# Kernel tuning notes

Measured on AMD Instinct MI355X. Metric: run time of the kernel, lower is better.

## Reference

```python
import jax, jax.numpy as jnp
import numpy as np

B, IN_DIM, UNITS = 16384, 3072, 3072  # batch, input_dim=3*unit1, units=3*unit2


def setup_inputs() -> dict:
    key = jax.random.key(0)
    k1, k2, k3 = jax.random.split(key, 3)
    inputs = jax.random.normal(k1, (B, IN_DIM), dtype=jnp.float32)
    # original init: uniform [0, 0.01) for w, zeros for b (gpe_bias = [0, 0])
    w = jax.random.uniform(k2, (IN_DIM, UNITS), dtype=jnp.float32, minval=0.0, maxval=0.01)
    b = jnp.zeros((UNITS,), dtype=jnp.float32)
    # per-unit binary diagonal mask, stored as [units, input_dim]
    mask = jax.random.randint(k3, (UNITS, IN_DIM), 0, 2, dtype=jnp.int32)
    return {"inputs": inputs, "w": w, "b": b, "mask": mask}


def reference(inputs, w, b, mask):
    # Original: p = transpose(s @ inputs^T, [2,0,1]) -> [batch, units, input_dim]
    #           f = diag_part(p @ w) + b            -> [batch, units]
    # Since s[u] = diag(mask[u]), this is exactly:
    #   f[b,u] = sum_i inputs[b,i] * mask[u,i] * w[i,u] + b[u]
    # i.e. a single masked GEMM with effective weight w * mask^T.
    w_eff = w * mask.T.astype(w.dtype)  # [input_dim, units]
    return inputs @ w_eff + b
```

## Files before the change

kernel.cpp:

```cpp
#include <hip/hip_runtime.h>

#define BATCH 16384
#define KDIM  3072
#define NDIM  3072

typedef __bf16 bf16;
typedef bf16  bf16x8  __attribute__((ext_vector_type(8)));
typedef float f32x16  __attribute__((ext_vector_type(16)));

__device__ __forceinline__ void g2l16(const bf16* g, bf16* l) {
    __builtin_amdgcn_global_load_lds(
        (__attribute__((address_space(1))) unsigned int*)g,
        (__attribute__((address_space(3))) unsigned int*)l,
        16, 0, 0);
}

__global__ __launch_bounds__(256) void cvt_a_kernel(const float* __restrict__ in,
                                                    bf16* __restrict__ out) {
    const long idx = (long)blockIdx.x * 256 + threadIdx.x;
    const float4* in4 = (const float4*)in;
    float4 a = in4[idx * 2];
    float4 b = in4[idx * 2 + 1];
    bf16x8 o;
    o[0] = (bf16)a.x; o[1] = (bf16)a.y; o[2] = (bf16)a.z; o[3] = (bf16)a.w;
    o[4] = (bf16)b.x; o[5] = (bf16)b.y; o[6] = (bf16)b.z; o[7] = (bf16)b.w;
    ((bf16x8*)out)[idx] = o;
}

__global__ __launch_bounds__(256) void weff_kernel(const float* __restrict__ w,
                                                   const int* __restrict__ mask,
                                                   bf16* __restrict__ wt) {
    __shared__ float tile[32][33];
    const int i0 = blockIdx.x * 32;
    const int u0 = blockIdx.y * 32;
    const int tx = threadIdx.x, ty = threadIdx.y;
#pragma unroll
    for (int r = 0; r < 4; r++)
        tile[ty + 8 * r][tx] = w[(long)(i0 + ty + 8 * r) * NDIM + u0 + tx];
    __syncthreads();
#pragma unroll
    for (int r = 0; r < 4; r++) {
        int u = u0 + ty + 8 * r;
        int i = i0 + tx;
        float v = tile[tx][ty + 8 * r] * (float)mask[(long)u * KDIM + i];
        wt[(long)u * KDIM + i] = (bf16)v;
    }
}

__global__ __launch_bounds__(256, 2) void gemm_kernel(const bf16* __restrict__ A,
                                                      const bf16* __restrict__ Bt,
                                                      const float* __restrict__ bias,
                                                      float* __restrict__ C) {
    __shared__ __align__(16) bf16 lds[2 * 12288];

    const int tid  = threadIdx.x;
    const int lane = tid & 63;
    const int wv   = tid >> 6;
    const long m0 = (long)blockIdx.y * 256;
    const long n0 = (long)blockIdx.x * 128;
    const int waveM = (wv >> 1) * 128;
    const int waveN = (wv & 1) * 64;

    const int srow   = tid >> 2;
    const int schunk = tid & 3;
    const bf16* gA = A + (m0 + srow) * KDIM + schunk * 8;
    const bf16* gB = Bt + (n0 + srow) * KDIM + schunk * 8;

    const int rl = lane & 31;
    const int kb = lane >> 5;
    const int aBase = (waveM + rl) * 32 + kb * 8;
    const int bBase = 8192 + (waveN + rl) * 32 + kb * 8;

    f32x16 acc[4][2] = {};

    {
        bf16* d = &lds[tid * 8];
#pragma unroll
        for (int j = 0; j < 4; j++) g2l16(gA + (long)(64 * j) * KDIM, d + j * 2048);
#pragma unroll
        for (int j = 0; j < 2; j++) g2l16(gB + (long)(64 * j) * KDIM, d + 8192 + j * 2048);
    }
    __syncthreads();

    for (int i = 0; i < KDIM / 32; ++i) {
        const int p = i & 1;
        if (i + 1 < KDIM / 32) {
            const long ko = (long)(i + 1) * 32;
            bf16* d = &lds[(1 - p) * 12288 + tid * 8];
#pragma unroll
            for (int j = 0; j < 4; j++) g2l16(gA + (long)(64 * j) * KDIM + ko, d + j * 2048);
#pragma unroll
            for (int j = 0; j < 2; j++) g2l16(gB + (long)(64 * j) * KDIM + ko, d + 8192 + j * 2048);
        }

        const bf16* bp = &lds[p * 12288];
#pragma unroll
        for (int t = 0; t < 2; t++) {
            bf16x8 a[4], b[2];
#pragma unroll
            for (int mi = 0; mi < 4; mi++)
                a[mi] = *(const bf16x8*)(bp + aBase + mi * 1024 + t * 16);
#pragma unroll
            for (int ni = 0; ni < 2; ni++)
                b[ni] = *(const bf16x8*)(bp + bBase + ni * 1024 + t * 16);
#pragma unroll
            for (int mi = 0; mi < 4; mi++)
#pragma unroll
                for (int ni = 0; ni < 2; ni++)
                    acc[mi][ni] = __builtin_amdgcn_mfma_f32_32x32x16_bf16(
                        a[mi], b[ni], acc[mi][ni], 0, 0, 0);
        }
        __syncthreads();
    }

#pragma unroll
    for (int mi = 0; mi < 4; mi++) {
#pragma unroll
        for (int ni = 0; ni < 2; ni++) {
            const long col   = n0 + waveN + ni * 32 + rl;
            const long rbase = m0 + waveM + mi * 32 + 4 * kb;
            const float bv = bias[col];
#pragma unroll
            for (int g = 0; g < 4; g++)
#pragma unroll
                for (int t = 0; t < 4; t++)
                    C[(rbase + 8 * g + t) * NDIM + col] = acc[mi][ni][4 * g + t] + bv;
        }
    }
}

__global__ __launch_bounds__(256) void naive_kernel(const float* __restrict__ x,
                                                    const float* __restrict__ w,
                                                    const float* __restrict__ bias,
                                                    const int* __restrict__ mask,
                                                    float* __restrict__ out) {
    const long idx = (long)blockIdx.x * 256 + threadIdx.x;
    const long bi = idx / NDIM;
    const int u = (int)(idx % NDIM);
    float s = 0.f;
    for (int k = 0; k < KDIM; k++)
        s += x[bi * KDIM + k] * w[(long)k * NDIM + u] * (float)mask[(long)u * KDIM + k];
    out[idx] = s + bias[u];
}

extern "C" void kernel_launch(void* const* d_in, const int* in_sizes, int n_in,
                              void* d_out, int out_size, void* d_ws, size_t ws_size,
                              hipStream_t stream) {
    const float* x    = (const float*)d_in[0];
    const float* w    = (const float*)d_in[1];
    const float* bias = (const float*)d_in[2];
    const int*   mask = (const int*)d_in[3];
    float* out = (float*)d_out;

    const size_t needA = (size_t)BATCH * KDIM * sizeof(bf16);
    const size_t needW = (size_t)NDIM * KDIM * sizeof(bf16);

    if (ws_size < needA + needW) {
        const long total = (long)BATCH * NDIM;
        naive_kernel<<<(int)(total / 256), 256, 0, stream>>>(x, w, bias, mask, out);
        return;
    }

    bf16* Abf = (bf16*)d_ws;
    bf16* Wt  = (bf16*)((char*)d_ws + needA);

    cvt_a_kernel<<<(BATCH * (KDIM / 8)) / 256, 256, 0, stream>>>(x, Abf);
    weff_kernel<<<dim3(KDIM / 32, NDIM / 32), dim3(32, 8), 0, stream>>>(w, mask, Wt);
    gemm_kernel<<<dim3(NDIM / 128, BATCH / 256), 256, 0, stream>>>(Abf, Wt, bias, out);
}
```

Measured before the change: 697.0 us.

## Enlarge GEMM tile to 256x256 with swizzled LDS, K=64 stages and XCD remap

The GEMM kernel moves to 512-thread blocks computing 256x256 output tiles with BK=64. Each tile is double-buffered in 128KB of LDS, with XOR-swizzled layout to avoid bank conflicts. Fragment loads are register double-buffered across k-substeps, MFMA issue runs under raised priority, and manual vmcnt waits plus barriers replace __syncthreads. Block ids are remapped so consecutive tiles spread across XCDs for better L2 reuse. The larger tile cuts global/LDS traffic per flop, but the LDS footprint limits occupancy to one block per CU despite launch bounds asking for two.

```diff
diff --git a/kernel.cpp b/kernel.cpp
--- a/kernel.cpp
+++ b/kernel.cpp
@@ -47,83 +47,119 @@
     }
 }
 
-__global__ __launch_bounds__(256, 2) void gemm_kernel(const bf16* __restrict__ A,
+__global__ __launch_bounds__(512, 2) void gemm_kernel(const bf16* __restrict__ A,
                                                       const bf16* __restrict__ Bt,
                                                       const float* __restrict__ bias,
                                                       float* __restrict__ C) {
-    __shared__ __align__(16) bf16 lds[2 * 12288];
+    __shared__ __align__(16) bf16 lds[2 * 32768];
 
     const int tid  = threadIdx.x;
     const int lane = tid & 63;
     const int wv   = tid >> 6;
-    const long m0 = (long)blockIdx.y * 256;
-    const long n0 = (long)blockIdx.x * 128;
-    const int waveM = (wv >> 1) * 128;
-    const int waveN = (wv & 1) * 64;
-
-    const int srow   = tid >> 2;
-    const int schunk = tid & 3;
-    const bf16* gA = A + (m0 + srow) * KDIM + schunk * 8;
-    const bf16* gB = Bt + (n0 + srow) * KDIM + schunk * 8;
-
-    const int rl = lane & 31;
-    const int kb = lane >> 5;
-    const int aBase = (waveM + rl) * 32 + kb * 8;
-    const int bBase = 8192 + (waveN + rl) * 32 + kb * 8;
+    const int rl   = lane & 31;
+    const int kb   = lane >> 5;
+    const int sx   = rl & 7;
+
+    const int lid = blockIdx.y * gridDim.x + blockIdx.x;
+    const int sid = (lid & 7) * 96 + (lid >> 3);
+    const long m0 = (long)(sid / 12) * 256;
+    const long n0 = (long)(sid % 12) * 256;
+
+    const int waveM = (wv >> 2) * 128;
+    const int waveN = (wv & 3) * 64;
+
+    const int srow = tid >> 3;
+    const int sc   = (tid & 7) ^ (srow & 7);
+    const bf16* gA = A  + (m0 + srow) * KDIM + sc * 8;
+    const bf16* gB = Bt + (n0 + srow) * KDIM + sc * 8;
+    bf16* const dA = &lds[tid * 8];
+    bf16* const dB = &lds[16384 + tid * 8];
+
+    const int aBase = (waveM + rl) * 64;
+    const int bBase = 16384 + (waveN + rl) * 64;
 
     f32x16 acc[4][2] = {};
 
-    {
-        bf16* d = &lds[tid * 8];
-#pragma unroll
-        for (int j = 0; j < 4; j++) g2l16(gA + (long)(64 * j) * KDIM, d + j * 2048);
-#pragma unroll
-        for (int j = 0; j < 2; j++) g2l16(gB + (long)(64 * j) * KDIM, d + 8192 + j * 2048);
-    }
-    __syncthreads();
-
-    for (int i = 0; i < KDIM / 32; ++i) {
+    auto STAGE = [&](int p, int kt) {
+        const long ko = (long)kt * 64;
+        bf16* da = dA + p * 32768;
+        bf16* db = dB + p * 32768;
+#pragma unroll
+        for (int j = 0; j < 4; ++j) g2l16(gA + (long)(64 * j) * KDIM + ko, da + j * 4096);
+#pragma unroll
+        for (int j = 0; j < 4; ++j) g2l16(gB + (long)(64 * j) * KDIM + ko, db + j * 4096);
+    };
+
+    auto COMPUTE = [&](const bf16* bp) {
+        bf16x8 af[2][4], bfr[2][2];
+        {
+            const int c = kb ^ sx;
+#pragma unroll
+            for (int mi = 0; mi < 4; ++mi)
+                af[0][mi] = *(const bf16x8*)(bp + aBase + mi * 2048 + c * 8);
+#pragma unroll
+            for (int ni = 0; ni < 2; ++ni)
+                bfr[0][ni] = *(const bf16x8*)(bp + bBase + ni * 2048 + c * 8);
+        }
+#pragma unroll
+        for (int ks = 0; ks < 4; ++ks) {
+            const int cur = ks & 1, nxt = cur ^ 1;
+            if (ks < 3) {
+                const int c = ((ks + 1) * 2 + kb) ^ sx;
+#pragma unroll
+                for (int mi = 0; mi < 4; ++mi)
+                    af[nxt][mi] = *(const bf16x8*)(bp + aBase + mi * 2048 + c * 8);
+#pragma unroll
+                for (int ni = 0; ni < 2; ++ni)
+                    bfr[nxt][ni] = *(const bf16x8*)(bp + bBase + ni * 2048 + c * 8);
+            }
+            __builtin_amdgcn_s_setprio(1);
+#pragma unroll
+            for (int mi = 0; mi < 4; ++mi)
+#pragma unroll
+                for (int ni = 0; ni < 2; ++ni)
+                    acc[mi][ni] = __builtin_amdgcn_mfma_f32_32x32x16_bf16(
+                        af[cur][mi], bfr[cur][ni], acc[mi][ni], 0, 0, 0);
+            __builtin_amdgcn_s_setprio(0);
+        }
+    };
+
+    const int NT = KDIM / 64;
+    STAGE(0, 0);
+    STAGE(1, 1);
+
+#pragma unroll 2
+    for (int i = 0; i < NT - 2; ++i) {
         const int p = i & 1;
-        if (i + 1 < KDIM / 32) {
-            const long ko = (long)(i + 1) * 32;
-            bf16* d = &lds[(1 - p) * 12288 + tid * 8];
-#pragma unroll
-            for (int j = 0; j < 4; j++) g2l16(gA + (long)(64 * j) * KDIM + ko, d + j * 2048);
-#pragma unroll
-            for (int j = 0; j < 2; j++) g2l16(gB + (long)(64 * j) * KDIM + ko, d + 8192 + j * 2048);
-        }
-
-        const bf16* bp = &lds[p * 12288];
-#pragma unroll
-        for (int t = 0; t < 2; t++) {
-            bf16x8 a[4], b[2];
-#pragma unroll
-            for (int mi = 0; mi < 4; mi++)
-                a[mi] = *(const bf16x8*)(bp + aBase + mi * 1024 + t * 16);
-#pragma unroll
-            for (int ni = 0; ni < 2; ni++)
-                b[ni] = *(const bf16x8*)(bp + bBase + ni * 1024 + t * 16);
-#pragma unroll
-            for (int mi = 0; mi < 4; mi++)
-#pragma unroll
-                for (int ni = 0; ni < 2; ni++)
-                    acc[mi][ni] = __builtin_amdgcn_mfma_f32_32x32x16_bf16(
-                        a[mi], b[ni], acc[mi][ni], 0, 0, 0);
-        }
-        __syncthreads();
-    }
-
-#pragma unroll
-    for (int mi = 0; mi < 4; mi++) {
-#pragma unroll
-        for (int ni = 0; ni < 2; ni++) {
-            const long col   = n0 + waveN + ni * 32 + rl;
+        asm volatile("s_waitcnt vmcnt(8)" ::: "memory");
+        __builtin_amdgcn_s_barrier();
+        asm volatile("" ::: "memory");
+        COMPUTE(&lds[p * 32768]);
+        asm volatile("s_waitcnt lgkmcnt(0)" ::: "memory");
+        __builtin_amdgcn_s_barrier();
+        asm volatile("" ::: "memory");
+        STAGE(p, i + 2);
+    }
+    asm volatile("s_waitcnt vmcnt(8)" ::: "memory");
+    __builtin_amdgcn_s_barrier();
+    asm volatile("" ::: "memory");
+    COMPUTE(&lds[0]);
+    asm volatile("s_waitcnt vmcnt(0)" ::: "memory");
+    __builtin_amdgcn_s_barrier();
+    asm volatile("" ::: "memory");
+    COMPUTE(&lds[32768]);
+
+#pragma unroll
+    for (int ni = 0; ni < 2; ++ni) {
+        const long col = n0 + waveN + ni * 32 + rl;
+        const float bv = bias[col];
+#pragma unroll
+        for (int mi = 0; mi < 4; ++mi) {
             const long rbase = m0 + waveM + mi * 32 + 4 * kb;
-            const float bv = bias[col];
-#pragma unroll
-            for (int g = 0; g < 4; g++)
-#pragma unroll
-                for (int t = 0; t < 4; t++)
+#pragma unroll
+            for (int g = 0; g < 4; ++g)
+#pragma unroll
+                for (int t = 0; t < 4; ++t)
                     C[(rbase + 8 * g + t) * NDIM + col] = acc[mi][ni][4 * g + t] + bv;
         }
     }
@@ -166,5 +202,5 @@
 
     cvt_a_kernel<<<(BATCH * (KDIM / 8)) / 256, 256, 0, stream>>>(x, Abf);
     weff_kernel<<<dim3(KDIM / 32, NDIM / 32), dim3(32, 8), 0, stream>>>(w, mask, Wt);
-    gemm_kernel<<<dim3(NDIM / 128, BATCH / 256), 256, 0, stream>>>(Abf, Wt, bias, out);
-}
+    gemm_kernel<<<dim3(NDIM / 256, BATCH / 256), 512, 0, stream>>>(Abf, Wt, bias, out);
+}
```

New measurement: 690.0 us. No clear change (-1.0%).
